# Optimization experiments

Hardware: AMD Instinct MI355X
Metric: run time of the kernel (lower is better)

Reference implementation:

```python
import jax, jax.numpy as jnp
import numpy as np

WINDOW = 48
RES = 50
PRED = 96

def setup_inputs() -> dict:
    key = jax.random.key(0)
    k1, k2, k3, k4, k5 = jax.random.split(key, 5)
    x = jax.random.normal(k1, (2048, 4800, 1), dtype=jnp.float32)
    W_lin = jax.random.normal(k2, (WINDOW, WINDOW), dtype=jnp.float32) * 0.1
    # W_in = inv(P) @ B with P orthogonal, B ~ U(-1,1); statistically a dense random matrix
    W_in = jax.random.uniform(k3, (RES, WINDOW), dtype=jnp.float32, minval=-1.0, maxval=1.0)
    # diagonal reservoir weights d ~ U(-0.95, 0.95)
    d = jax.random.uniform(k4, (RES,), dtype=jnp.float32, minval=-0.95, maxval=0.95)
    W_out = jax.random.normal(k5, (PRED, RES), dtype=jnp.float32) * 0.1
    return {"x": x, "W_lin": W_lin, "W_in": W_in, "d": d, "W_out": W_out}

def reference(x, W_lin, W_in, d, W_out):
    B, S, C = x.shape  # C == 1 (non-individual path requires squeeze(1))
    seg = S // WINDOW
    # permute(0,2,1) -> view(B, C, seg, WINDOW) -> squeeze(1)
    u = x[..., 0].reshape(B, seg, WINDOW)
    # input linear (no bias): u @ W_lin.T
    u = jnp.einsum('bsw,vw->bsv', u, W_lin)
    # input projection into reservoir: W_in @ u_t for every step (one big GEMM)
    v = jnp.einsum('bsw,rw->bsr', u, W_in)  # [B, seg, RES]
    # ESN state persists across the batch loop too (never reset in update_state),
    # so the recurrence is one serial chain over B*seg steps.
    v_flat = v.reshape(B * seg, RES)
    def step(state, vt):
        # activation is LeakyReLU(negative_slope=1.0) == identity
        new = vt + d * state
        return new, new
    _, states = jax.lax.scan(step, jnp.zeros((RES,), dtype=v.dtype), v_flat)
    states = states.reshape(B, seg, RES)
    last = states[:, -1, :]              # [B, RES]
    out = last @ W_out.T                 # [B, PRED]
    return out[:, :, None]               # unsqueeze(1).permute(0,2,1) -> [B, PRED, 1]
```

## Files before the change

### kernel.cpp

```cpp
#include <hip/hip_runtime.h>

#define WINDOW 48
#define RES 50
#define PRED 96
#define BATCH 2048
#define KTOT 4800
#define KTRUNC 12
#define KS 10
#define KRB 512
#define ASTR 516

typedef __attribute__((ext_vector_type(8))) short short8v;
typedef __attribute__((ext_vector_type(4))) float f32x4;
typedef __attribute__((ext_vector_type(4))) int i32x4;

#define OFF_DK 0
#define OFF_WT 800
#define OFF_M  5600
#define OFF_KS 8000
#define OFF_LP 171840

__device__ __forceinline__ float ipow(float b, int n) {
    float r = 1.f, p = b;
    while (n) { if (n & 1) r *= p; p *= p; n >>= 1; }
    return r;
}

__device__ __forceinline__ unsigned pack2bf(float v0, float v1) {
    unsigned u0 = __builtin_bit_cast(unsigned, v0);
    unsigned u1 = __builtin_bit_cast(unsigned, v1);
    unsigned t0 = u0 + 0x7FFFu + ((u0 >> 16) & 1u);
    unsigned t1 = u1 + 0x7FFFu + ((u1 >> 16) & 1u);
    return (t0 >> 16) | (t1 & 0xFFFF0000u);
}

__global__ __launch_bounds__(256) void k0a(const float* __restrict__ W_lin,
                                           const float* __restrict__ W_in,
                                           const float* __restrict__ d,
                                           const float* __restrict__ W_out,
                                           float* __restrict__ ws) {
    int f = blockIdx.x * 256 + threadIdx.x;
    if (f < 2400) {
        int r = f / WINDOW, w = f % WINDOW;
        float acc = 0.f;
        for (int v = 0; v < WINDOW; ++v)
            acc = fmaf(W_in[r * WINDOW + v], W_lin[v * WINDOW + w], acc);
        ws[OFF_M + f] = acc;
    } else if (f < 3200) {
        int e = f - 2400;
        int k = e / RES, r = e % RES;
        ws[OFF_DK + e] = ipow(ipow(d[r], 100), k);
    } else if (f < 8000) {
        int e = f - 3200;
        int r = e / PRED, o = e % PRED;
        ws[OFF_WT + e] = W_out[o * RES + r];
    }
}

__global__ __launch_bounds__(256) void k0b(const float* __restrict__ d,
                                           float* __restrict__ ws) {
    unsigned idx = blockIdx.x * 256 + threadIdx.x;
    int j = idx & 7;
    int l = (idx >> 3) & 63;
    int n = (idx >> 9) & 3;
    int K = idx >> 11;
    int c = n * 16 + (l & 15);
    int k = K * 32 + ((l >> 4) << 3) + j;
    float val = 0.f;
    if (c < RES && k < KTOT) {
        int jj = k / WINDOW, w = k - jj * WINDOW;
        val = ipow(d[c], 99 - jj) * ws[OFF_M + c * WINDOW + w];
    }
    unsigned u = __builtin_bit_cast(unsigned, val);
    ((unsigned short*)(ws + OFF_KS))[idx] =
        (unsigned short)((u + 0x7FFFu + ((u >> 16) & 1u)) >> 16);
}

__global__ __launch_bounds__(256, 3) void k1(const float* __restrict__ x,
                                             const float* __restrict__ ws,
                                             float* __restrict__ lp) {
    __shared__ float S[16 * ASTR];
    const unsigned short* KbSw = (const unsigned short*)(ws + OFF_KS);
    int bid = blockIdx.x;
    int mt = bid / KS, ks = bid - mt * KS;
    int b0 = mt * 16, kb = ks * KRB;
    int t = threadIdx.x, w = t >> 6, l = t & 63;
    int row16 = l & 15, kq = l >> 4;

#pragma unroll
    for (int i = 0; i < 8; ++i) {
        int e = t + i * 256;
        int row = e >> 7, q = e & 127;
        float4 v = make_float4(0.f, 0.f, 0.f, 0.f);
        if (kb + 4 * q < KTOT)
            v = *(const float4*)(x + (size_t)(b0 + row) * KTOT + kb + 4 * q);
        *(float4*)(S + row * ASTR + 4 * q) = v;
    }
    __syncthreads();

    int K0 = ks * 16 + w * 4;
    const unsigned short* bbase = KbSw + (size_t)K0 * 2048 + l * 8;
    short8v B0[4], B1[4], B2[4], B3[4];
#pragma unroll
    for (int st = 0; st < 4; ++st) {
        B0[st] = *(const short8v*)(bbase + st * 2048);
        B1[st] = *(const short8v*)(bbase + st * 2048 + 512);
        B2[st] = *(const short8v*)(bbase + st * 2048 + 1024);
        B3[st] = *(const short8v*)(bbase + st * 2048 + 1536);
    }

    f32x4 acc0 = (f32x4)(0.f), acc1 = (f32x4)(0.f), acc2 = (f32x4)(0.f), acc3 = (f32x4)(0.f);
    const float* abase = S + row16 * ASTR + w * 128 + kq * 8;

#pragma unroll
    for (int st = 0; st < 4; ++st) {
        f32x4 a0 = *(const f32x4*)(abase + st * 32);
        f32x4 a1 = *(const f32x4*)(abase + st * 32 + 4);
        i32x4 wv;
        wv[0] = (int)pack2bf(a0[0], a0[1]);
        wv[1] = (int)pack2bf(a0[2], a0[3]);
        wv[2] = (int)pack2bf(a1[0], a1[1]);
        wv[3] = (int)pack2bf(a1[2], a1[3]);
        short8v av = __builtin_bit_cast(short8v, wv);
        acc0 = __builtin_amdgcn_mfma_f32_16x16x32_bf16(av, B0[st], acc0, 0, 0, 0);
        acc1 = __builtin_amdgcn_mfma_f32_16x16x32_bf16(av, B1[st], acc1, 0, 0, 0);
        acc2 = __builtin_amdgcn_mfma_f32_16x16x32_bf16(av, B2[st], acc2, 0, 0, 0);
        acc3 = __builtin_amdgcn_mfma_f32_16x16x32_bf16(av, B3[st], acc3, 0, 0, 0);
    }
    __syncthreads();

    float* Ps = S + w * 1088;
#pragma unroll
    for (int i = 0; i < 4; ++i) {
        int rr = (kq * 4 + i) * 68;
        Ps[rr + row16]      = acc0[i];
        Ps[rr + row16 + 16] = acc1[i];
        Ps[rr + row16 + 32] = acc2[i];
        Ps[rr + row16 + 48] = acc3[i];
    }
    __syncthreads();

#pragma unroll
    for (int i = 0; i < 4; ++i) {
        int o = t + i * 256;
        int r = o >> 6, c = o & 63;
        if (c < RES) {
            float sum = (S[r * 68 + c] + S[1088 + r * 68 + c])
                      + (S[2176 + r * 68 + c] + S[3264 + r * 68 + c]);
            lp[((size_t)ks * BATCH + b0 + r) * 50 + c] = sum;
        }
    }
}

__global__ __launch_bounds__(256) void k2(const float* __restrict__ ws,
                                          float* __restrict__ out) {
    __shared__ float Ls[27 * 52];
    __shared__ float Ss[16 * 52];
    const float* lp = ws + OFF_LP;
    const float* Dk = ws + OFF_DK;
    const float* Wt = ws + OFF_WT;
    int B0 = blockIdx.x * 16;
    int t = threadIdx.x;

    for (int e = t; e < 27 * 50; e += 256) {
        int lr = e / 50, c = e - lr * 50;
        int bb = B0 - 11 + lr;
        float sum = 0.f;
        if (bb >= 0) {
#pragma unroll
            for (int sp = 0; sp < KS; ++sp)
                sum += lp[((size_t)sp * BATCH + bb) * 50 + c];
        }
        Ls[lr * 52 + c] = sum;
    }
    __syncthreads();

    for (int e = t; e < 16 * 50; e += 256) {
        int i = e / 50, r = e - i * 50;
        float acc = 0.f;
#pragma unroll
        for (int k = 0; k < KTRUNC; ++k)
            acc = fmaf(Dk[k * RES + r], Ls[(11 + i - k) * 52 + r], acc);
        Ss[i * 52 + r] = acc;
    }
    __syncthreads();

    for (int e = t; e < 16 * PRED; e += 256) {
        int i = e / PRED, o = e - i * PRED;
        float acc = 0.f;
#pragma unroll 10
        for (int r = 0; r < RES; ++r)
            acc = fmaf(Ss[i * 52 + r], Wt[r * PRED + o], acc);
        out[(B0 + i) * PRED + o] = acc;
    }
}

extern "C" void kernel_launch(void* const* d_in, const int* in_sizes, int n_in,
                              void* d_out, int out_size, void* d_ws, size_t ws_size,
                              hipStream_t stream) {
    const float* x     = (const float*)d_in[0];
    const float* W_lin = (const float*)d_in[1];
    const float* W_in  = (const float*)d_in[2];
    const float* d     = (const float*)d_in[3];
    const float* W_out = (const float*)d_in[4];
    float* out = (float*)d_out;
    float* ws  = (float*)d_ws;
    float* lp  = ws + OFF_LP;

    k0a<<<32, 256, 0, stream>>>(W_lin, W_in, d, W_out, ws);
    k0b<<<1280, 256, 0, stream>>>(d, ws);
    k1<<<128 * KS, 256, 0, stream>>>(x, ws, lp);
    k2<<<128, 256, 0, stream>>>(ws, out);
}
```

Measured before the change: 36.01 us.

## Precompute decay powers table, hoist B loads, split final reduction into two kernels

Adds a precomputed table of d^(99-j) in k0a so k0b reads a value instead of running a per-element ipow loop. The weight-fragment global loads in k1 move ahead of the x staging so they overlap with it. The old k2 is split in two: k2a sums the split-K partials as a vectorized reduction, and k2b runs one block per batch row for the truncated recurrence and the output projection. This removes the redundant recomputation of halo rows and raises parallelism in the tail. The cost is an extra kernel launch and an extra workspace round trip.

```diff
diff --git a/kernel.cpp b/kernel.cpp
--- a/kernel.cpp
+++ b/kernel.cpp
@@ -14,11 +14,13 @@
 typedef __attribute__((ext_vector_type(4))) float f32x4;
 typedef __attribute__((ext_vector_type(4))) int i32x4;
 
-#define OFF_DK 0
-#define OFF_WT 800
-#define OFF_M  5600
-#define OFF_KS 8000
-#define OFF_LP 171840
+#define OFF_M  0
+#define OFF_DJ 2400
+#define OFF_DK 8800
+#define OFF_WT 9600
+#define OFF_KS 14400
+#define OFF_LP 178240
+#define OFF_L  1202240
 
 __device__ __forceinline__ float ipow(float b, int n) {
     float r = 1.f, p = b;
@@ -42,22 +44,29 @@
     int f = blockIdx.x * 256 + threadIdx.x;
     if (f < 2400) {
         int r = f / WINDOW, w = f % WINDOW;
-        float acc = 0.f;
-        for (int v = 0; v < WINDOW; ++v)
-            acc = fmaf(W_in[r * WINDOW + v], W_lin[v * WINDOW + w], acc);
-        ws[OFF_M + f] = acc;
-    } else if (f < 3200) {
+        float a0 = 0.f, a1 = 0.f;
+#pragma unroll
+        for (int v = 0; v < WINDOW; v += 2) {
+            a0 = fmaf(W_in[r * WINDOW + v],     W_lin[v * WINDOW + w],       a0);
+            a1 = fmaf(W_in[r * WINDOW + v + 1], W_lin[(v + 1) * WINDOW + w], a1);
+        }
+        ws[OFF_M + f] = a0 + a1;
+    } else if (f < 8800) {
         int e = f - 2400;
+        int j = e >> 6, r = e & 63;
+        ws[OFF_DJ + e] = (r < RES) ? ipow(d[r], 99 - j) : 0.f;
+    } else if (f < 9600) {
+        int e = f - 8800;
         int k = e / RES, r = e % RES;
         ws[OFF_DK + e] = ipow(ipow(d[r], 100), k);
-    } else if (f < 8000) {
-        int e = f - 3200;
+    } else if (f < 14400) {
+        int e = f - 9600;
         int r = e / PRED, o = e % PRED;
         ws[OFF_WT + e] = W_out[o * RES + r];
     }
 }
 
-__global__ __launch_bounds__(256) void k0b(const float* __restrict__ d,
+__global__ __launch_bounds__(256) void k0b(const float* __restrict__ ws_c,
                                            float* __restrict__ ws) {
     unsigned idx = blockIdx.x * 256 + threadIdx.x;
     int j = idx & 7;
@@ -69,7 +78,7 @@
     float val = 0.f;
     if (c < RES && k < KTOT) {
         int jj = k / WINDOW, w = k - jj * WINDOW;
-        val = ipow(d[c], 99 - jj) * ws[OFF_M + c * WINDOW + w];
+        val = ws_c[OFF_DJ + (jj << 6) + c] * ws_c[OFF_M + c * WINDOW + w];
     }
     unsigned u = __builtin_bit_cast(unsigned, val);
     ((unsigned short*)(ws + OFF_KS))[idx] =
@@ -87,6 +96,17 @@
     int t = threadIdx.x, w = t >> 6, l = t & 63;
     int row16 = l & 15, kq = l >> 4;
 
+    int K0 = ks * 16 + w * 4;
+    const unsigned short* bbase = KbSw + (size_t)K0 * 2048 + l * 8;
+    short8v B0[4], B1[4], B2[4], B3[4];
+#pragma unroll
+    for (int st = 0; st < 4; ++st) {
+        B0[st] = *(const short8v*)(bbase + st * 2048);
+        B1[st] = *(const short8v*)(bbase + st * 2048 + 512);
+        B2[st] = *(const short8v*)(bbase + st * 2048 + 1024);
+        B3[st] = *(const short8v*)(bbase + st * 2048 + 1536);
+    }
+
 #pragma unroll
     for (int i = 0; i < 8; ++i) {
         int e = t + i * 256;
@@ -98,20 +118,8 @@
     }
     __syncthreads();
 
-    int K0 = ks * 16 + w * 4;
-    const unsigned short* bbase = KbSw + (size_t)K0 * 2048 + l * 8;
-    short8v B0[4], B1[4], B2[4], B3[4];
-#pragma unroll
-    for (int st = 0; st < 4; ++st) {
-        B0[st] = *(const short8v*)(bbase + st * 2048);
-        B1[st] = *(const short8v*)(bbase + st * 2048 + 512);
-        B2[st] = *(const short8v*)(bbase + st * 2048 + 1024);
-        B3[st] = *(const short8v*)(bbase + st * 2048 + 1536);
-    }
-
     f32x4 acc0 = (f32x4)(0.f), acc1 = (f32x4)(0.f), acc2 = (f32x4)(0.f), acc3 = (f32x4)(0.f);
     const float* abase = S + row16 * ASTR + w * 128 + kq * 8;
-
 #pragma unroll
     for (int st = 0; st < 4; ++st) {
         f32x4 a0 = *(const f32x4*)(abase + st * 32);
@@ -139,7 +147,6 @@
         Ps[rr + row16 + 48] = acc3[i];
     }
     __syncthreads();
-
 #pragma unroll
     for (int i = 0; i < 4; ++i) {
         int o = t + i * 256;
@@ -152,46 +159,40 @@
     }
 }
 
-__global__ __launch_bounds__(256) void k2(const float* __restrict__ ws,
-                                          float* __restrict__ out) {
-    __shared__ float Ls[27 * 52];
-    __shared__ float Ss[16 * 52];
-    const float* lp = ws + OFF_LP;
+__global__ __launch_bounds__(256) void k2a(float* __restrict__ ws) {
+    int e = blockIdx.x * 256 + threadIdx.x;
+    const f32x4* lp4 = (const f32x4*)(ws + OFF_LP);
+    f32x4 sum = lp4[e];
+#pragma unroll
+    for (int sp = 1; sp < KS; ++sp)
+        sum += lp4[(size_t)sp * 25600 + e];
+    ((f32x4*)(ws + OFF_L))[e] = sum;
+}
+
+__global__ __launch_bounds__(128) void k2b(const float* __restrict__ ws,
+                                           float* __restrict__ out) {
+    const float* L  = ws + OFF_L;
     const float* Dk = ws + OFF_DK;
     const float* Wt = ws + OFF_WT;
-    int B0 = blockIdx.x * 16;
+    __shared__ float s_s[52];
+    int b = blockIdx.x;
     int t = threadIdx.x;
-
-    for (int e = t; e < 27 * 50; e += 256) {
-        int lr = e / 50, c = e - lr * 50;
-        int bb = B0 - 11 + lr;
-        float sum = 0.f;
-        if (bb >= 0) {
-#pragma unroll
-            for (int sp = 0; sp < KS; ++sp)
-                sum += lp[((size_t)sp * BATCH + bb) * 50 + c];
+    if (t < RES) {
+        float acc = 0.f;
+#pragma unroll
+        for (int k = 0; k < KTRUNC; ++k) {
+            int bb = b - k;
+            if (bb >= 0) acc = fmaf(Dk[k * RES + t], L[(size_t)bb * 50 + t], acc);
         }
-        Ls[lr * 52 + c] = sum;
-    }
-    __syncthreads();
-
-    for (int e = t; e < 16 * 50; e += 256) {
-        int i = e / 50, r = e - i * 50;
-        float acc = 0.f;
-#pragma unroll
-        for (int k = 0; k < KTRUNC; ++k)
-            acc = fmaf(Dk[k * RES + r], Ls[(11 + i - k) * 52 + r], acc);
-        Ss[i * 52 + r] = acc;
-    }
-    __syncthreads();
-
-    for (int e = t; e < 16 * PRED; e += 256) {
-        int i = e / PRED, o = e - i * PRED;
+        s_s[t] = acc;
+    }
+    __syncthreads();
+    if (t < PRED) {
         float acc = 0.f;
 #pragma unroll 10
         for (int r = 0; r < RES; ++r)
-            acc = fmaf(Ss[i * 52 + r], Wt[r * PRED + o], acc);
-        out[(B0 + i) * PRED + o] = acc;
+            acc = fmaf(s_s[r], Wt[r * PRED + t], acc);
+        out[b * PRED + t] = acc;
     }
 }
 
@@ -207,8 +208,9 @@
     float* ws  = (float*)d_ws;
     float* lp  = ws + OFF_LP;
 
-    k0a<<<32, 256, 0, stream>>>(W_lin, W_in, d, W_out, ws);
-    k0b<<<1280, 256, 0, stream>>>(d, ws);
+    k0a<<<57, 256, 0, stream>>>(W_lin, W_in, d, W_out, ws);
+    k0b<<<1280, 256, 0, stream>>>(ws, ws);
     k1<<<128 * KS, 256, 0, stream>>>(x, ws, lp);
-    k2<<<128, 256, 0, stream>>>(ws, out);
-}
+    k2a<<<100, 256, 0, stream>>>(ws);
+    k2b<<<BATCH, 128, 0, stream>>>(ws, out);
+}
```

New measurement: 33.12 us. 1.09x faster.
